# Kernel tuning notes

Measured on AMD Instinct MI355X. Metric: run time of the kernel, lower is better.

The kernel has to match this reference:

```python
import jax, jax.numpy as jnp
import numpy as np

GROUPS = 256   # == planes (default groups=None -> planes)
NODE_NUM = 32
EPS = 1e-5


def setup_inputs() -> dict:
    key = jax.random.key(0)
    ks = jax.random.split(key, 12)
    b, cin, planes, h, w = 4, 512, 256, 128, 128
    node_fea = planes // NODE_NUM  # 8
    inp = {
        "x": jax.random.normal(ks[0], (b, cin, h, w), jnp.float32),
        "Wt": jax.random.normal(ks[1], (planes, cin), jnp.float32) * 0.02,
        "Wp": jax.random.normal(ks[2], (planes, cin), jnp.float32) * 0.02,
        "Wg": jax.random.normal(ks[3], (planes, cin), jnp.float32) * 0.02,
        "Wz": jax.random.normal(ks[4], (cin,), jnp.float32) * 0.1,  # grouped 1x1 conv, 1 in-ch per group
        "W_adj": jax.random.normal(ks[5], (NODE_NUM, NODE_NUM), jnp.float32) * 0.1,
        "bn_adj_gamma": jnp.ones((NODE_NUM,), jnp.float32),
        "bn_adj_beta": jnp.zeros((NODE_NUM,), jnp.float32),
        "bn_adj_mean": jax.random.normal(ks[6], (NODE_NUM,), jnp.float32) * 0.1,
        "bn_adj_var": jax.random.uniform(ks[7], (NODE_NUM,), jnp.float32) + 0.5,
        "W_wg": jax.random.normal(ks[8], (node_fea, node_fea), jnp.float32) * 0.1,
        "bn_wg_gamma": jnp.ones((node_fea,), jnp.float32),
        "bn_wg_beta": jnp.zeros((node_fea,), jnp.float32),
        "bn_wg_mean": jax.random.normal(ks[9], (node_fea,), jnp.float32) * 0.1,
        "bn_wg_var": jax.random.uniform(ks[10], (node_fea,), jnp.float32) + 0.5,
        "gn_gamma": jnp.ones((cin,), jnp.float32),
        "gn_beta": jnp.zeros((cin,), jnp.float32),
    }
    return inp


def _bn1d_eval(z, mean, var, gamma, beta):
    # BatchNorm1d over channel dim 1 of [b, C, L], eval mode (running stats)
    inv = jax.lax.rsqrt(var + EPS)
    return (z - mean[:, None]) * (inv * gamma)[:, None] + beta[:, None]


def reference(x, Wt, Wp, Wg, Wz, W_adj, bn_adj_gamma, bn_adj_beta, bn_adj_mean,
              bn_adj_var, W_wg, bn_wg_gamma, bn_wg_beta, bn_wg_mean, bn_wg_var,
              gn_gamma, gn_beta):
    b, cin, h, w = x.shape
    # 1x1 convs t/p/g
    t = jnp.einsum('bihw,oi->bohw', x, Wt)
    p = jnp.einsum('bihw,oi->bohw', x, Wp)
    g = jnp.einsum('bihw,oi->bohw', x, Wg)
    planes = t.shape[1]
    node_fea = planes // NODE_NUM
    # per-group dot-product kernel: replaces the Python loop of tiny bmms.
    # _c = planes // GROUPS channels per group; att[b, gidx] = sum(p_g * g_g)
    att = jnp.sum((p * g).reshape(b, GROUPS, -1), axis=-1)  # [b, groups]
    # split(dim=1, node_num) + cat(dim=2): z_idt[b, i, k] = att[b, k*node_num + i]
    z_idt = att.reshape(b, GROUPS // NODE_NUM, NODE_NUM).transpose(0, 2, 1)  # [b, node_num, node_fea]
    # node-adjacency conv (Conv1d k=1 over node dim) + BN + ReLU + residual
    z = jnp.einsum('nm,bmf->bnf', W_adj, z_idt)
    z = _bn1d_eval(z, bn_adj_mean, bn_adj_var, bn_adj_gamma, bn_adj_beta)
    z = jax.nn.relu(z) + z_idt
    # feature conv on transposed layout + BN + ReLU
    z = z.transpose(0, 2, 1)  # [b, node_fea, node_num]
    z = jnp.einsum('fe,ben->bfn', W_wg, z)
    z = _bn1d_eval(z, bn_wg_mean, bn_wg_var, bn_wg_gamma, bn_wg_beta)
    z = jax.nn.relu(z).transpose(0, 2, 1)  # [b, node_num, node_fea]
    # reshape to per-channel scalars and gate t
    zvec = z.reshape(b, planes)[:, :, None, None]  # [b, planes, 1, 1]
    xg = zvec * t  # [b, planes, h, w]
    # grouped 1x1 conv z: groups=planes, 1 input ch / group, r=cin//planes out ch / group
    r = cin // planes
    y = Wz[None, :, None, None] * jnp.repeat(xg, r, axis=1)  # [b, cin, h, w]
    # GroupNorm(num_groups=GROUPS, num_channels=cin)
    yg = y.reshape(b, GROUPS, -1)  # each group: (cin//GROUPS)*h*w elements
    mean = yg.mean(axis=-1, keepdims=True)
    var = yg.var(axis=-1, keepdims=True)
    yn = ((yg - mean) * jax.lax.rsqrt(var + EPS)).reshape(b, cin, h, w)
    yn = yn * gn_gamma[None, :, None, None] + gn_beta[None, :, None, None]
    return yn + x
```

## Files before the change

### kernel.cpp

```cpp
#include <hip/hip_runtime.h>

#define HW 16384
#define CIN 512
#define PL 256
#define EPSF 1e-5f
#define SLO 0.0009765625f

using half8  = __attribute__((ext_vector_type(8))) _Float16;
using half4v = __attribute__((ext_vector_type(4))) _Float16;
using f32x4  = __attribute__((ext_vector_type(4))) float;

__device__ inline void gload_lds16(const void* g, void* l) {
  __builtin_amdgcn_global_load_lds((const __attribute__((address_space(1))) void*)g,
                                   (__attribute__((address_space(3))) void*)l, 16, 0, 0);
}

__global__ __launch_bounds__(256) void k_conv(const float* __restrict__ x,
                                              _Float16* __restrict__ Xh,
                                              _Float16* __restrict__ Xl,
                                              float* __restrict__ xsum) {
  __shared__ float ws4[4];
  int row = blockIdx.x;
  int tid = threadIdx.x;
  const float* xr = x + ((size_t)row << 14);
  _Float16* hr = Xh + ((size_t)row << 14);
  _Float16* lr = Xl + ((size_t)row << 14);
  float s = 0.f;
#pragma unroll
  for (int j = 0; j < 8; ++j) {
    int o = j * 2048 + tid * 8;
    float4 v0 = *reinterpret_cast<const float4*>(xr + o);
    float4 v1 = *reinterpret_cast<const float4*>(xr + o + 4);
    half8 h, l;
    h[0] = (_Float16)v0.x; h[1] = (_Float16)v0.y; h[2] = (_Float16)v0.z; h[3] = (_Float16)v0.w;
    h[4] = (_Float16)v1.x; h[5] = (_Float16)v1.y; h[6] = (_Float16)v1.z; h[7] = (_Float16)v1.w;
    l[0] = (_Float16)((v0.x - (float)h[0]) * 1024.f);
    l[1] = (_Float16)((v0.y - (float)h[1]) * 1024.f);
    l[2] = (_Float16)((v0.z - (float)h[2]) * 1024.f);
    l[3] = (_Float16)((v0.w - (float)h[3]) * 1024.f);
    l[4] = (_Float16)((v1.x - (float)h[4]) * 1024.f);
    l[5] = (_Float16)((v1.y - (float)h[5]) * 1024.f);
    l[6] = (_Float16)((v1.z - (float)h[6]) * 1024.f);
    l[7] = (_Float16)((v1.w - (float)h[7]) * 1024.f);
    *reinterpret_cast<half8*>(hr + o) = h;
    *reinterpret_cast<half8*>(lr + o) = l;
    s += v0.x + v0.y + v0.z + v0.w + v1.x + v1.y + v1.z + v1.w;
  }
#pragma unroll
  for (int m = 1; m < 64; m <<= 1) s += __shfl_xor(s, m);
  if ((tid & 63) == 0) ws4[tid >> 6] = s;
  __syncthreads();
  if (tid == 0) xsum[row] = ws4[0] + ws4[1] + ws4[2] + ws4[3];
}

__global__ __launch_bounds__(256, 4) void k_gx(const _Float16* __restrict__ Xh,
                                               const _Float16* __restrict__ Xl,
                                               float* __restrict__ GH,
                                               float* __restrict__ C1,
                                               _Float16* __restrict__ xT) {
  __shared__ char smem[32768];
  int tid = threadIdx.x;

  if (blockIdx.x < 832) {
    _Float16* lA = (_Float16*)smem;
    _Float16* lB = (_Float16*)(smem + 16384);
    int wg = blockIdx.x;
    int id = (wg & 7) * 104 + (wg >> 3);
    int b = id / 208;
    int rem = id % 208;
    int ks = rem / 26;
    int u = rem % 26;
    int chain, ti, tj;
    if (u < 10) {
      chain = 0;
      ti = 0;
      while ((ti + 1) * (ti + 2) / 2 <= u) ++ti;
      tj = u - ti * (ti + 1) / 2;
    } else {
      chain = 1;
      int t = u - 10;
      ti = t >> 2; tj = t & 3;
    }
    int wave = tid >> 6, lane = tid & 63, l15 = lane & 15, l4 = lane >> 4;
    int wr = wave >> 1, wc = wave & 1;
    const _Float16* Asrc = (chain ? Xl : Xh) + (size_t)b * CIN * HW;
    const _Float16* Bsrc = Xh + (size_t)b * CIN * HW;
    float* D = chain ? C1 : GH;

    int srow = lane >> 3;
    int sgran = (lane & 7) ^ (srow & 7);
    int kbase = ks << 11;
    const _Float16* gA[4];
    const _Float16* gB[4];
#pragma unroll
    for (int i = 0; i < 4; ++i) {
      int row = i * 32 + wave * 8 + srow;
      gA[i] = Asrc + (size_t)(ti * 128 + row) * HW + kbase + sgran * 8;
      gB[i] = Bsrc + (size_t)(tj * 128 + row) * HW + kbase + sgran * 8;
    }
    char* ldA = (char*)lA + wave * 1024;
    char* ldB = (char*)lB + wave * 1024;

    int adA[4][2], adB[4][2];
#pragma unroll
    for (int rf = 0; rf < 4; ++rf) {
      int r = wr * 64 + rf * 16 + l15;
#pragma unroll
      for (int ksub = 0; ksub < 2; ++ksub)
        adA[rf][ksub] = r * 128 + (((ksub * 4 + l4) ^ (r & 7)) << 4);
    }
#pragma unroll
    for (int cf = 0; cf < 4; ++cf) {
      int c = wc * 64 + cf * 16 + l15;
#pragma unroll
      for (int ksub = 0; ksub < 2; ++ksub)
        adB[cf][ksub] = c * 128 + (((ksub * 4 + l4) ^ (c & 7)) << 4);
    }

    f32x4 acc[4][4];
#pragma unroll
    for (int rf = 0; rf < 4; ++rf)
#pragma unroll
      for (int cf = 0; cf < 4; ++cf) acc[rf][cf] = f32x4{0.f, 0.f, 0.f, 0.f};

    for (int s = 0; s < 32; ++s) {
      int ko = s * 64;
#pragma unroll
      for (int i = 0; i < 4; ++i) {
        gload_lds16(gA[i] + ko, ldA + i * 4096);
        gload_lds16(gB[i] + ko, ldB + i * 4096);
      }
      __syncthreads();
#pragma unroll
      for (int ksub = 0; ksub < 2; ++ksub) {
        half8 af[4], bf[4];
#pragma unroll
        for (int rf = 0; rf < 4; ++rf)
          af[rf] = *reinterpret_cast<const half8*>((char*)lA + adA[rf][ksub]);
#pragma unroll
        for (int cf = 0; cf < 4; ++cf)
          bf[cf] = *reinterpret_cast<const half8*>((char*)lB + adB[cf][ksub]);
#pragma unroll
        for (int rf = 0; rf < 4; ++rf)
#pragma unroll
          for (int cf = 0; cf < 4; ++cf)
            acc[rf][cf] = __builtin_amdgcn_mfma_f32_16x16x32_f16(af[rf], bf[cf], acc[rf][cf], 0, 0, 0);
      }
      __syncthreads();
    }

    size_t bo = (size_t)b << 18;
#pragma unroll
    for (int rf = 0; rf < 4; ++rf)
#pragma unroll
      for (int cf = 0; cf < 4; ++cf)
#pragma unroll
        for (int r = 0; r < 4; ++r) {
          int i = ti * 128 + wr * 64 + rf * 16 + l4 * 4 + r;
          int j = tj * 128 + wc * 64 + cf * 16 + l15;
          atomicAdd(D + bo + ((size_t)i << 9) + j, acc[rf][cf][r]);
        }
  } else {
    _Float16* lds = (_Float16*)smem;
    int bid = blockIdx.x - 832;
    int hw0 = (bid & 255) << 6;
    int c0 = ((bid >> 8) & 7) << 6;
    int b = bid >> 11;
    int rl = tid >> 3, seg = tid & 7;
    const _Float16* hb = Xh + ((size_t)b << 23);
#pragma unroll
    for (int pass = 0; pass < 2; ++pass) {
      int cl = pass * 32 + rl;
      int chunk = cl >> 3, wi = cl & 7;
      half8 v = *reinterpret_cast<const half8*>(hb + ((size_t)(c0 + cl) << 14) + hw0 + seg * 8);
#pragma unroll
      for (int e = 0; e < 8; ++e) {
        int r = seg * 8 + e;
        lds[r * 72 + ((chunk ^ ((r >> 3) & 7)) << 3) + wi] = v[e];
      }
    }
    __syncthreads();
    _Float16* tb = xT + (((size_t)b << 14) + hw0) * CIN + c0;
#pragma unroll
    for (int pass = 0; pass < 2; ++pass) {
      int hwl = pass * 32 + rl;
      int chp = seg ^ ((hwl >> 3) & 7);
      half8 o = *reinterpret_cast<const half8*>(&lds[hwl * 72 + (chp << 3)]);
      *reinterpret_cast<half8*>(tb + (size_t)hwl * CIN + seg * 8) = o;
    }
  }
}

__global__ __launch_bounds__(256) void k_sym(const float* __restrict__ GH,
                                             const float* __restrict__ C1,
                                             float* __restrict__ Gs) {
  __shared__ float T1[64 * 65];
  __shared__ float TG[64 * 65];
  int I = blockIdx.x, J = blockIdx.y, b = blockIdx.z;
  int i0 = I << 6, j0 = J << 6;
  bool upper = (I >> 1) >= (J >> 1);
  size_t bo = (size_t)b << 18;
  int tid = threadIdx.x;
  int r = tid >> 2, cs = (tid & 3) << 4;
#pragma unroll
  for (int u = 0; u < 16; u += 4) {
    size_t toff = bo + (((size_t)(j0 + r)) << 9) + i0 + cs + u;
    float4 v = *reinterpret_cast<const float4*>(C1 + toff);
    T1[r * 65 + cs + u + 0] = v.x; T1[r * 65 + cs + u + 1] = v.y;
    T1[r * 65 + cs + u + 2] = v.z; T1[r * 65 + cs + u + 3] = v.w;
    if (!upper) {
      float4 g = *reinterpret_cast<const float4*>(GH + toff);
      TG[r * 65 + cs + u + 0] = g.x; TG[r * 65 + cs + u + 1] = g.y;
      TG[r * 65 + cs + u + 2] = g.z; TG[r * 65 + cs + u + 3] = g.w;
    }
  }
  __syncthreads();
#pragma unroll
  for (int u = 0; u < 16; u += 4) {
    size_t off = bo + (((size_t)(i0 + r)) << 9) + j0 + cs + u;
    float4 c = *reinterpret_cast<const float4*>(C1 + off);
    float t0 = T1[(cs + u + 0) * 65 + r];
    float t1 = T1[(cs + u + 1) * 65 + r];
    float t2 = T1[(cs + u + 2) * 65 + r];
    float t3 = T1[(cs + u + 3) * 65 + r];
    float4 o;
    if (upper) {
      float4 h = *reinterpret_cast<const float4*>(GH + off);
      o.x = h.x + SLO * (c.x + t0);
      o.y = h.y + SLO * (c.y + t1);
      o.z = h.z + SLO * (c.z + t2);
      o.w = h.w + SLO * (c.w + t3);
    } else {
      o.x = TG[(cs + u + 0) * 65 + r] + SLO * (c.x + t0);
      o.y = TG[(cs + u + 1) * 65 + r] + SLO * (c.y + t1);
      o.z = TG[(cs + u + 2) * 65 + r] + SLO * (c.z + t2);
      o.w = TG[(cs + u + 3) * 65 + r] + SLO * (c.w + t3);
    }
    *reinterpret_cast<float4*>(Gs + off) = o;
  }
}

__global__ __launch_bounds__(256) void k_V(const float* __restrict__ Gs,
                                           const float* __restrict__ Wg,
                                           const float* __restrict__ Wt,
                                           float* __restrict__ V) {
  __shared__ float Gl[64 * 65];
  __shared__ float Wl[64 * 65];
  int it = blockIdx.x, ot = blockIdx.y, b = blockIdx.z;
  int i0 = it << 6, o0 = ot << 6;
  int tid = threadIdx.x;
  int srow = tid >> 2, sseg = (tid & 3) << 4;
  const float* gsb = Gs + ((size_t)b << 18);
  int orow = o0 + srow;
  const float* wrow = (orow < 256) ? (Wg + (size_t)orow * 512) : (Wt + (size_t)(orow - 256) * 512);
  float acc[4][4];
#pragma unroll
  for (int a = 0; a < 4; ++a)
#pragma unroll
    for (int c = 0; c < 4; ++c) acc[a][c] = 0.f;
  int oy = (tid >> 4) << 2, ix = (tid & 15) << 2;
  for (int jc = 0; jc < 512; jc += 64) {
    __syncthreads();
#pragma unroll
    for (int u = 0; u < 16; u += 4) {
      float4 g = *reinterpret_cast<const float4*>(gsb + ((size_t)(i0 + srow) << 9) + jc + sseg + u);
      float4 w = *reinterpret_cast<const float4*>(wrow + jc + sseg + u);
      Gl[srow * 65 + sseg + u + 0] = g.x; Gl[srow * 65 + sseg + u + 1] = g.y;
      Gl[srow * 65 + sseg + u + 2] = g.z; Gl[srow * 65 + sseg + u + 3] = g.w;
      Wl[srow * 65 + sseg + u + 0] = w.x; Wl[srow * 65 + sseg + u + 1] = w.y;
      Wl[srow * 65 + sseg + u + 2] = w.z; Wl[srow * 65 + sseg + u + 3] = w.w;
    }
    __syncthreads();
    for (int j = 0; j < 64; ++j) {
      float w0 = Wl[(oy + 0) * 65 + j], w1 = Wl[(oy + 1) * 65 + j];
      float w2 = Wl[(oy + 2) * 65 + j], w3 = Wl[(oy + 3) * 65 + j];
      float g0 = Gl[(ix + 0) * 65 + j], g1 = Gl[(ix + 1) * 65 + j];
      float g2 = Gl[(ix + 2) * 65 + j], g3 = Gl[(ix + 3) * 65 + j];
      acc[0][0] += w0 * g0; acc[0][1] += w0 * g1; acc[0][2] += w0 * g2; acc[0][3] += w0 * g3;
      acc[1][0] += w1 * g0; acc[1][1] += w1 * g1; acc[1][2] += w1 * g2; acc[1][3] += w1 * g3;
      acc[2][0] += w2 * g0; acc[2][1] += w2 * g1; acc[2][2] += w2 * g2; acc[2][3] += w2 * g3;
      acc[3][0] += w3 * g0; acc[3][1] += w3 * g1; acc[3][2] += w3 * g2; acc[3][3] += w3 * g3;
    }
  }
  float* vb = V + ((size_t)b << 18);
#pragma unroll
  for (int a = 0; a < 4; ++a) {
    float4 vv = {acc[a][0], acc[a][1], acc[a][2], acc[a][3]};
    *reinterpret_cast<float4*>(vb + ((size_t)(o0 + oy + a) << 9) + i0 + ix) = vv;
  }
}

__global__ __launch_bounds__(256) void k_red2(const float* __restrict__ V,
                                              const float* __restrict__ xsum,
                                              const float* __restrict__ Wp,
                                              const float* __restrict__ Wt,
                                              float* __restrict__ att,
                                              float* __restrict__ tsum,
                                              float* __restrict__ tsq) {
  int blk = blockIdx.x;
  int b = blk >> 4;
  int og = (blk & 15) << 4;
  int tid = threadIdx.x;
  int ol = tid >> 4, seg = tid & 15;
  int o = og + ol;
  const float* vg = V + ((size_t)b << 18) + ((size_t)o << 9) + seg * 32;
  const float* vt = V + ((size_t)b << 18) + ((size_t)(256 + o) << 9) + seg * 32;
  const float* wp = Wp + (size_t)o * 512 + seg * 32;
  const float* wt = Wt + (size_t)o * 512 + seg * 32;
  const float* xs = xsum + b * CIN + seg * 32;
  float sa = 0.f, sq = 0.f, sm = 0.f;
#pragma unroll
  for (int i = 0; i < 32; i += 4) {
    float4 a = *reinterpret_cast<const float4*>(vg + i);
    float4 p = *reinterpret_cast<const float4*>(wp + i);
    float4 c = *reinterpret_cast<const float4*>(vt + i);
    float4 t = *reinterpret_cast<const float4*>(wt + i);
    float4 s = *reinterpret_cast<const float4*>(xs + i);
    sa += a.x * p.x + a.y * p.y + a.z * p.z + a.w * p.w;
    sq += c.x * t.x + c.y * t.y + c.z * t.z + c.w * t.w;
    sm += t.x * s.x + t.y * s.y + t.z * s.z + t.w * s.w;
  }
#pragma unroll
  for (int m = 1; m < 16; m <<= 1) {
    sa += __shfl_xor(sa, m);
    sq += __shfl_xor(sq, m);
    sm += __shfl_xor(sm, m);
  }
  if (seg == 0) {
    att[b * PL + o] = sa;
    tsq[b * PL + o] = sq;
    tsum[b * PL + o] = sm;
  }
}

__global__ __launch_bounds__(1024) void k_graph(
    const float* __restrict__ att, const float* __restrict__ tsum, const float* __restrict__ tsq,
    const float* __restrict__ W_adj, const float* __restrict__ bnag, const float* __restrict__ bnab,
    const float* __restrict__ bnam, const float* __restrict__ bnav,
    const float* __restrict__ W_wg, const float* __restrict__ bwgg, const float* __restrict__ bwgb,
    const float* __restrict__ bwgm, const float* __restrict__ bwgv,
    const float* __restrict__ Wz, const float* __restrict__ gng, const float* __restrict__ gnb,
    float* __restrict__ sA, float* __restrict__ sB) {
  __shared__ float att_l[4 * 256];
  __shared__ float z_l[4 * 256];
  __shared__ float zv_l[4 * 256];
  int tid = threadIdx.x;
  att_l[tid] = att[tid];
  __syncthreads();
  int b = tid >> 8, r = tid & 255, i = r >> 3, k = r & 7;
  float z1 = 0.f;
#pragma unroll
  for (int m = 0; m < 32; ++m) z1 += W_adj[i * 32 + m] * att_l[b * 256 + k * 32 + m];
  float inv = rsqrtf(bnav[i] + EPSF);
  float z = (z1 - bnam[i]) * inv * bnag[i] + bnab[i];
  z = fmaxf(z, 0.f) + att_l[b * 256 + k * 32 + i];
  z_l[b * 256 + i * 8 + k] = z;
  __syncthreads();
  float z2 = 0.f;
#pragma unroll
  for (int e = 0; e < 8; ++e) z2 += W_wg[k * 8 + e] * z_l[b * 256 + i * 8 + e];
  float inv2 = rsqrtf(bwgv[k] + EPSF);
  z2 = (z2 - bwgm[k]) * inv2 * bwgg[k] + bwgb[k];
  zv_l[b * 256 + i * 8 + k] = fmaxf(z2, 0.f);
  __syncthreads();
  int g = r;
  float s = zv_l[b * 256 + g];
  float m1 = tsum[b * 256 + g] * (1.f / 16384.f);
  float m2 = tsq[b * 256 + g] * (1.f / 16384.f);
  float a0 = Wz[2 * g] * s, a1 = Wz[2 * g + 1] * s;
  float mu = 0.5f * (a0 + a1) * m1;
  float ey2 = 0.5f * (a0 * a0 + a1 * a1) * m2;
  float var = ey2 - mu * mu;
  float invg = rsqrtf(var + EPSF);
  int c = b * CIN + 2 * g;
  sA[c]     = a0 * invg * gng[2 * g];
  sA[c + 1] = a1 * invg * gng[2 * g + 1];
  sB[c]     = gnb[2 * g]     - mu * invg * gng[2 * g];
  sB[c + 1] = gnb[2 * g + 1] - mu * invg * gng[2 * g + 1];
}

__global__ __launch_bounds__(256) void k_M(const float* __restrict__ Wt,
                                           const float* __restrict__ sA,
                                           _Float16* __restrict__ M) {
  int idx = blockIdx.x * 256 + threadIdx.x;
  int k8 = idx & 63;
  int c = (idx >> 6) & 511;
  int b = idx >> 15;
  float s = sA[b * 512 + c];
  const float* wrow = Wt + ((size_t)(c >> 1) << 9) + k8 * 8;
  int kbase = k8 * 8;
  half8 h;
#pragma unroll
  for (int j = 0; j < 8; ++j) {
    float v = s * wrow[j] + ((kbase + j) == c ? 1.f : 0.f);
    h[j] = (_Float16)v;
  }
  *reinterpret_cast<half8*>(M + (((size_t)(b * 512 + c)) << 9) + kbase) = h;
}

__global__ __launch_bounds__(256, 4) void k_tout(const _Float16* __restrict__ xT,
                                                 const _Float16* __restrict__ M,
                                                 const float* __restrict__ sB,
                                                 float* __restrict__ out) {
  __shared__ _Float16 lA[128 * 64];
  __shared__ _Float16 lB[128 * 64];
  int wg = blockIdx.x;
  int id = (wg & 7) * 256 + (wg >> 3);
  int b = id >> 9;
  int rem = id & 511;
  int ct = rem >> 7;
  int ht = rem & 127;
  int tid = threadIdx.x;
  int wave = tid >> 6, lane = tid & 63, l15 = lane & 15, l4 = lane >> 4;
  int wr = wave >> 1, wc = wave & 1;
  const _Float16* Mb = M + ((size_t)b << 18);
  const _Float16* xTb = xT + (size_t)b * HW * CIN;

  int srow = lane >> 3;
  int sgran = (lane & 7) ^ (srow & 7);
  const _Float16* gA[4];
  const _Float16* gB[4];
#pragma unroll
  for (int i = 0; i < 4; ++i) {
    int row = i * 32 + wave * 8 + srow;
    gA[i] = Mb + ((size_t)(ct * 128 + row) << 9) + sgran * 8;
    gB[i] = xTb + ((size_t)(ht * 128 + row) << 9) + sgran * 8;
  }
  char* ldA = (char*)lA + wave * 1024;
  char* ldB = (char*)lB + wave * 1024;

  int adA[4][2], adB[4][2];
#pragma unroll
  for (int rf = 0; rf < 4; ++rf) {
    int r = wr * 64 + rf * 16 + l15;
#pragma unroll
    for (int ksub = 0; ksub < 2; ++ksub)
      adA[rf][ksub] = r * 128 + (((ksub * 4 + l4) ^ (r & 7)) << 4);
  }
#pragma unroll
  for (int cf = 0; cf < 4; ++cf) {
    int c = wc * 64 + cf * 16 + l15;
#pragma unroll
    for (int ksub = 0; ksub < 2; ++ksub)
      adB[cf][ksub] = c * 128 + (((ksub * 4 + l4) ^ (c & 7)) << 4);
  }

  f32x4 acc[4][4];
#pragma unroll
  for (int rf = 0; rf < 4; ++rf)
#pragma unroll
    for (int cf = 0; cf < 4; ++cf) acc[rf][cf] = f32x4{0.f, 0.f, 0.f, 0.f};

  for (int s = 0; s < 8; ++s) {
    int ko = s * 64;
#pragma unroll
    for (int i = 0; i < 4; ++i) {
      gload_lds16(gA[i] + ko, ldA + i * 4096);
      gload_lds16(gB[i] + ko, ldB + i * 4096);
    }
    __syncthreads();
#pragma unroll
    for (int ksub = 0; ksub < 2; ++ksub) {
      half8 af[4], bf[4];
#pragma unroll
      for (int rf = 0; rf < 4; ++rf)
        af[rf] = *reinterpret_cast<const half8*>((char*)lA + adA[rf][ksub]);
#pragma unroll
      for (int cf = 0; cf < 4; ++cf)
        bf[cf] = *reinterpret_cast<const half8*>((char*)lB + adB[cf][ksub]);
#pragma unroll
      for (int rf = 0; rf < 4; ++rf)
#pragma unroll
        for (int cf = 0; cf < 4; ++cf)
          acc[rf][cf] = __builtin_amdgcn_mfma_f32_16x16x32_f16(af[rf], bf[cf], acc[rf][cf], 0, 0, 0);
    }
    __syncthreads();
  }

  size_t outb = ((size_t)b * CIN) << 14;
#pragma unroll
  for (int rf = 0; rf < 4; ++rf) {
#pragma unroll
    for (int r = 0; r < 4; ++r) {
      int c = ct * 128 + wr * 64 + rf * 16 + l4 * 4 + r;
      float bb = sB[b * CIN + c];
      size_t off = outb + ((size_t)c << 14) + ht * 128 + wc * 64 + l15;
#pragma unroll
      for (int cf = 0; cf < 4; ++cf)
        out[off + cf * 16] = acc[rf][cf][r] + bb;
    }
  }
}

extern "C" void kernel_launch(void* const* d_in, const int* in_sizes, int n_in,
                              void* d_out, int out_size, void* d_ws, size_t ws_size,
                              hipStream_t stream) {
  const float* x    = (const float*)d_in[0];
  const float* Wt   = (const float*)d_in[1];
  const float* Wp   = (const float*)d_in[2];
  const float* Wg   = (const float*)d_in[3];
  const float* Wz   = (const float*)d_in[4];
  const float* Wadj = (const float*)d_in[5];
  const float* bnag = (const float*)d_in[6];
  const float* bnab = (const float*)d_in[7];
  const float* bnam = (const float*)d_in[8];
  const float* bnav = (const float*)d_in[9];
  const float* Wwg  = (const float*)d_in[10];
  const float* bwgg = (const float*)d_in[11];
  const float* bwgb = (const float*)d_in[12];
  const float* bwgm = (const float*)d_in[13];
  const float* bwgv = (const float*)d_in[14];
  const float* gng  = (const float*)d_in[15];
  const float* gnb  = (const float*)d_in[16];

  char* ws = (char*)d_ws;
  _Float16* xT = (_Float16*)(ws);
  float* GH   = (float*)(ws + 67371008);
  float* C1   = (float*)(ws + 71565312);
  float* Gs   = (float*)(ws + 75759616);
  float* V    = (float*)(ws + 79953920);
  float* xsum = (float*)(ws + 84148224);
  float* att  = (float*)(ws + 84156416);
  float* tsum = (float*)(ws + 84160512);
  float* tsq  = (float*)(ws + 84164608);
  float* sA   = (float*)(ws + 84168704);
  float* sB   = (float*)(ws + 84176896);
  if (ws_size < (size_t)84185088) return;
  _Float16* M = (_Float16*)GH;

  _Float16* Xh = (_Float16*)((char*)d_out);
  _Float16* Xl = (_Float16*)((char*)d_out + 67108864);
  float* out = (float*)d_out;

  hipMemsetAsync(GH, 0, 8388608, stream);
  k_conv<<<dim3(2048), dim3(256), 0, stream>>>(x, Xh, Xl, xsum);
  k_gx<<<dim3(9024), dim3(256), 0, stream>>>(Xh, Xl, GH, C1, xT);
  k_sym<<<dim3(8, 8, 4), dim3(256), 0, stream>>>(GH, C1, Gs);
  k_V<<<dim3(8, 8, 4), dim3(256), 0, stream>>>(Gs, Wg, Wt, V);
  k_red2<<<dim3(64), dim3(256), 0, stream>>>(V, xsum, Wp, Wt, att, tsum, tsq);
  k_graph<<<dim3(1), dim3(1024), 0, stream>>>(att, tsum, tsq, Wadj, bnag, bnab, bnam, bnav,
                                              Wwg, bwgg, bwgb, bwgm, bwgv, Wz, gng, gnb, sA, sB);
  k_M<<<dim3(512), dim3(256), 0, stream>>>(Wt, sA, M);
  k_tout<<<dim3(2048), dim3(256), 0, stream>>>(xT, M, sB, out);
}
```

Before: 263.6 us.

## Double-buffer LDS tiles with prefetch two stages ahead in GEMM kernels

Both MFMA GEMM kernels (k_gx and k_tout) now use two 32KB LDS buffers. Global-to-LDS loads are issued two k-steps ahead, with explicit vmcnt waits and raw barriers replacing the load-then-syncthreads pattern, so memory latency overlaps MFMA compute. LDS per block doubles to 64KB and launch bounds drop to 2 blocks per CU, trading occupancy for intra-block overlap.

```diff
diff --git a/kernel.cpp b/kernel.cpp
--- a/kernel.cpp
+++ b/kernel.cpp
@@ -53,17 +53,15 @@
   if (tid == 0) xsum[row] = ws4[0] + ws4[1] + ws4[2] + ws4[3];
 }
 
-__global__ __launch_bounds__(256, 4) void k_gx(const _Float16* __restrict__ Xh,
+__global__ __launch_bounds__(256, 2) void k_gx(const _Float16* __restrict__ Xh,
                                                const _Float16* __restrict__ Xl,
                                                float* __restrict__ GH,
                                                float* __restrict__ C1,
                                                _Float16* __restrict__ xT) {
-  __shared__ char smem[32768];
+  __shared__ char smem[65536];
   int tid = threadIdx.x;
 
   if (blockIdx.x < 832) {
-    _Float16* lA = (_Float16*)smem;
-    _Float16* lB = (_Float16*)(smem + 16384);
     int wg = blockIdx.x;
     int id = (wg & 7) * 104 + (wg >> 3);
     int b = id / 208;
@@ -98,8 +96,6 @@
       gA[i] = Asrc + (size_t)(ti * 128 + row) * HW + kbase + sgran * 8;
       gB[i] = Bsrc + (size_t)(tj * 128 + row) * HW + kbase + sgran * 8;
     }
-    char* ldA = (char*)lA + wave * 1024;
-    char* ldB = (char*)lB + wave * 1024;
 
     int adA[4][2], adB[4][2];
 #pragma unroll
@@ -123,30 +119,51 @@
 #pragma unroll
       for (int cf = 0; cf < 4; ++cf) acc[rf][cf] = f32x4{0.f, 0.f, 0.f, 0.f};
 
+#pragma unroll
+    for (int p = 0; p < 2; ++p) {
+      char* dA = smem + (p << 15) + wave * 1024;
+      char* dB = smem + (p << 15) + 16384 + wave * 1024;
+      int ko = p * 64;
+#pragma unroll
+      for (int i = 0; i < 4; ++i) {
+        gload_lds16(gA[i] + ko, dA + i * 4096);
+        gload_lds16(gB[i] + ko, dB + i * 4096);
+      }
+    }
+
     for (int s = 0; s < 32; ++s) {
-      int ko = s * 64;
-#pragma unroll
-      for (int i = 0; i < 4; ++i) {
-        gload_lds16(gA[i] + ko, ldA + i * 4096);
-        gload_lds16(gB[i] + ko, ldB + i * 4096);
-      }
-      __syncthreads();
+      if (s == 31) asm volatile("s_waitcnt vmcnt(0)" ::: "memory");
+      else         asm volatile("s_waitcnt vmcnt(8)" ::: "memory");
+      __builtin_amdgcn_s_barrier();
+      char* cA = smem + ((s & 1) << 15);
+      char* cB = cA + 16384;
 #pragma unroll
       for (int ksub = 0; ksub < 2; ++ksub) {
         half8 af[4], bf[4];
 #pragma unroll
         for (int rf = 0; rf < 4; ++rf)
-          af[rf] = *reinterpret_cast<const half8*>((char*)lA + adA[rf][ksub]);
+          af[rf] = *reinterpret_cast<const half8*>(cA + adA[rf][ksub]);
 #pragma unroll
         for (int cf = 0; cf < 4; ++cf)
-          bf[cf] = *reinterpret_cast<const half8*>((char*)lB + adB[cf][ksub]);
+          bf[cf] = *reinterpret_cast<const half8*>(cB + adB[cf][ksub]);
 #pragma unroll
         for (int rf = 0; rf < 4; ++rf)
 #pragma unroll
           for (int cf = 0; cf < 4; ++cf)
             acc[rf][cf] = __builtin_amdgcn_mfma_f32_16x16x32_f16(af[rf], bf[cf], acc[rf][cf], 0, 0, 0);
       }
-      __syncthreads();
+      asm volatile("s_waitcnt lgkmcnt(0)" ::: "memory");
+      __builtin_amdgcn_s_barrier();
+      if (s + 2 < 32) {
+        int ko = (s + 2) * 64;
+        char* dA = smem + ((s & 1) << 15) + wave * 1024;
+        char* dB = smem + ((s & 1) << 15) + 16384 + wave * 1024;
+#pragma unroll
+        for (int i = 0; i < 4; ++i) {
+          gload_lds16(gA[i] + ko, dA + i * 4096);
+          gload_lds16(gB[i] + ko, dB + i * 4096);
+        }
+      }
     }
 
     size_t bo = (size_t)b << 18;
@@ -398,12 +415,11 @@
   *reinterpret_cast<half8*>(M + (((size_t)(b * 512 + c)) << 9) + kbase) = h;
 }
 
-__global__ __launch_bounds__(256, 4) void k_tout(const _Float16* __restrict__ xT,
+__global__ __launch_bounds__(256, 2) void k_tout(const _Float16* __restrict__ xT,
                                                  const _Float16* __restrict__ M,
                                                  const float* __restrict__ sB,
                                                  float* __restrict__ out) {
-  __shared__ _Float16 lA[128 * 64];
-  __shared__ _Float16 lB[128 * 64];
+  __shared__ char smem[65536];
   int wg = blockIdx.x;
   int id = (wg & 7) * 256 + (wg >> 3);
   int b = id >> 9;
@@ -426,8 +442,6 @@
     gA[i] = Mb + ((size_t)(ct * 128 + row) << 9) + sgran * 8;
     gB[i] = xTb + ((size_t)(ht * 128 + row) << 9) + sgran * 8;
   }
-  char* ldA = (char*)lA + wave * 1024;
-  char* ldB = (char*)lB + wave * 1024;
 
   int adA[4][2], adB[4][2];
 #pragma unroll
@@ -451,30 +465,51 @@
 #pragma unroll
     for (int cf = 0; cf < 4; ++cf) acc[rf][cf] = f32x4{0.f, 0.f, 0.f, 0.f};
 
+#pragma unroll
+  for (int p = 0; p < 2; ++p) {
+    char* dA = smem + (p << 15) + wave * 1024;
+    char* dB = smem + (p << 15) + 16384 + wave * 1024;
+    int ko = p * 64;
+#pragma unroll
+    for (int i = 0; i < 4; ++i) {
+      gload_lds16(gA[i] + ko, dA + i * 4096);
+      gload_lds16(gB[i] + ko, dB + i * 4096);
+    }
+  }
+
   for (int s = 0; s < 8; ++s) {
-    int ko = s * 64;
-#pragma unroll
-    for (int i = 0; i < 4; ++i) {
-      gload_lds16(gA[i] + ko, ldA + i * 4096);
-      gload_lds16(gB[i] + ko, ldB + i * 4096);
-    }
-    __syncthreads();
+    if (s == 7) asm volatile("s_waitcnt vmcnt(0)" ::: "memory");
+    else        asm volatile("s_waitcnt vmcnt(8)" ::: "memory");
+    __builtin_amdgcn_s_barrier();
+    char* cA = smem + ((s & 1) << 15);
+    char* cB = cA + 16384;
 #pragma unroll
     for (int ksub = 0; ksub < 2; ++ksub) {
       half8 af[4], bf[4];
 #pragma unroll
       for (int rf = 0; rf < 4; ++rf)
-        af[rf] = *reinterpret_cast<const half8*>((char*)lA + adA[rf][ksub]);
+        af[rf] = *reinterpret_cast<const half8*>(cA + adA[rf][ksub]);
 #pragma unroll
       for (int cf = 0; cf < 4; ++cf)
-        bf[cf] = *reinterpret_cast<const half8*>((char*)lB + adB[cf][ksub]);
+        bf[cf] = *reinterpret_cast<const half8*>(cB + adB[cf][ksub]);
 #pragma unroll
       for (int rf = 0; rf < 4; ++rf)
 #pragma unroll
         for (int cf = 0; cf < 4; ++cf)
           acc[rf][cf] = __builtin_amdgcn_mfma_f32_16x16x32_f16(af[rf], bf[cf], acc[rf][cf], 0, 0, 0);
     }
-    __syncthreads();
+    asm volatile("s_waitcnt lgkmcnt(0)" ::: "memory");
+    __builtin_amdgcn_s_barrier();
+    if (s + 2 < 8) {
+      int ko = (s + 2) * 64;
+      char* dA = smem + ((s & 1) << 15) + wave * 1024;
+      char* dB = smem + ((s & 1) << 15) + 16384 + wave * 1024;
+#pragma unroll
+      for (int i = 0; i < 4; ++i) {
+        gload_lds16(gA[i] + ko, dA + i * 4096);
+        gload_lds16(gB[i] + ko, dB + i * 4096);
+      }
+    }
   }
 
   size_t outb = ((size_t)b * CIN) << 14;
```

New measurement: 266.2 us. About the same (+1.0%).
